# Kernel tuning notes

Measured on AMD Instinct MI355X. Metric: run time of the kernel, lower is better.

## Reference

```python
import jax, jax.numpy as jnp
import numpy as np

B, N, DIM, H = 4, 2048, 1024, 16
HEAD_DIM = DIM // H
SCALE = HEAD_DIM ** -0.5


def setup_inputs() -> dict:
    key = jax.random.key(0)
    k1, k2, k3 = jax.random.split(key, 3)
    x = jax.random.normal(k1, (B, N, DIM), dtype=jnp.float32)
    w_qkv = jax.random.normal(k2, (DIM, 3 * DIM), dtype=jnp.float32) * (DIM ** -0.5)
    w_proj = jax.random.normal(k3, (DIM, DIM), dtype=jnp.float32) * (DIM ** -0.5)
    b_proj = jnp.zeros((DIM,), dtype=jnp.float32)
    return {"x": x, "w_qkv": w_qkv, "w_proj": w_proj, "b_proj": b_proj}


def reference(x, w_qkv, w_proj, b_proj):
    Bs, Ns, C = x.shape
    qkv = x @ w_qkv                       # [B, N, 3C]
    q, k, v = jnp.split(qkv, 3, axis=-1)
    # [B, N, C] -> [B, H, N, D]
    def heads(t):
        return t.reshape(Bs, Ns, H, HEAD_DIM).transpose(0, 2, 1, 3)
    q, k, v = heads(q), heads(k), heads(v)
    attn = jnp.einsum('bhnd,bhmd->bhnm', q, k) * SCALE
    attn = jax.nn.softmax(attn, axis=-1)
    out = jnp.einsum('bhnm,bhmd->bhnd', attn, v)
    out = out.transpose(0, 2, 1, 3).reshape(Bs, Ns, C)
    return out @ w_proj + b_proj
```

## Files before the change

### kernel.cpp

```cpp
#include <hip/hip_runtime.h>
#include <hip/hip_bf16.h>


typedef short bf16x8 __attribute__((ext_vector_type(8)));
typedef float f32x4  __attribute__((ext_vector_type(4)));

#define BN   4
#define SEQ  2048
#define CDIM 1024
#define NH   16
#define HD   64
#define QKVN 3072
#define MTOT 8192
#define QSCALE_LOG2E 0.18033688011112042f

static __device__ __forceinline__ unsigned short f2bf(float f){
    union { float f; unsigned int i; } v; v.f = f;
    unsigned int r = v.i + 0x7FFFu + ((v.i >> 16) & 1u);
    return (unsigned short)(r >> 16);
}

static __device__ __forceinline__ unsigned int pk2bf(float a, float b){
#if __has_builtin(__builtin_amdgcn_cvt_pk_bf16_f32)
    auto r = __builtin_amdgcn_cvt_pk_bf16_f32(a, b);
    unsigned int u; __builtin_memcpy(&u, &r, 4); return u;
#else
    return (unsigned int)f2bf(a) | ((unsigned int)f2bf(b) << 16);
#endif
}

static __device__ __forceinline__ float fast_exp2(float x){
#if __has_builtin(__builtin_amdgcn_exp2f)
    return __builtin_amdgcn_exp2f(x);
#else
    return __expf(x * 0.69314718055994531f);
#endif
}

typedef __attribute__((address_space(3))) unsigned int        as3_uint;
typedef const __attribute__((address_space(1))) unsigned int  as1_uint;
static __device__ __forceinline__ void load_lds16(
    const unsigned short* g, unsigned short* l)
{
    __builtin_amdgcn_global_load_lds((as1_uint*)g, (as3_uint*)l, 16, 0, 0);
}

__global__ __launch_bounds__(256) void convert_f32_bf16(
    const float* __restrict__ in, unsigned short* __restrict__ out)
{
    size_t i = ((size_t)blockIdx.x * 256 + threadIdx.x) * 8;
    f32x4 a = *(const f32x4*)(in + i);
    f32x4 b = *(const f32x4*)(in + i + 4);
    union { unsigned int u[4]; bf16x8 v; } o;
    o.u[0] = pk2bf(a[0], a[1]); o.u[1] = pk2bf(a[2], a[3]);
    o.u[2] = pk2bf(b[0], b[1]); o.u[3] = pk2bf(b[2], b[3]);
    *(bf16x8*)(out + i) = o.v;
}

__global__ __launch_bounds__(256) void transpose_f32_to_bf16(
    const float* __restrict__ in, unsigned short* __restrict__ out,
    int in_rs, int out_rs)
{
    __shared__ unsigned short tile[32][33];
    int c0 = blockIdx.x * 32, r0 = blockIdx.y * 32;
    int tx = threadIdx.x, ty = threadIdx.y;
    #pragma unroll
    for (int j = 0; j < 4; j++)
        tile[ty + 8*j][tx] = f2bf(in[(long long)(r0 + ty + 8*j) * in_rs + c0 + tx]);
    __syncthreads();
    #pragma unroll
    for (int j = 0; j < 4; j++)
        out[(long long)(c0 + ty + 8*j) * out_rs + r0 + tx] = tile[tx][ty + 8*j];
}

__global__ __launch_bounds__(256) void pack_k(
    const unsigned short* __restrict__ qkv, unsigned short* __restrict__ kvpack)
{
    int blk = blockIdx.x;
    int bh = blk >> 6, t = blk & 63;
    int b = bh >> 4, h = bh & 15;
    int tid = threadIdx.x;
    int fr = tid >> 6, l = tid & 63;
    int quad = l >> 4, l15 = l & 15;
    int tb = fr >> 1, d32 = (fr & 1) * 32;
    int row = b*SEQ + t*32 + (l15 >> 2)*8 + (l15 & 3) + 4*tb;
    bf16x8 v = *(const bf16x8*)(qkv + (size_t)row * QKVN + CDIM + h*HD + d32 + quad*8);
    *(bf16x8*)(kvpack + ((size_t)blk*8 + fr)*512 + (size_t)l*8) = v;
}

__global__ __launch_bounds__(256) void pack_v(
    const unsigned short* __restrict__ qkv, unsigned short* __restrict__ vpack)
{
    __shared__ unsigned short tile[32][66];
    int blk = blockIdx.x;
    int bh = blk >> 6, t = blk & 63;
    int b = bh >> 4, h = bh & 15;
    int tid = threadIdx.x;
    int kk = tid >> 3, dd8 = (tid & 7) * 8;
    bf16x8 v = *(const bf16x8*)(qkv + (size_t)(b*SEQ + t*32 + kk) * QKVN
                                + 2*CDIM + h*HD + dd8);
    #pragma unroll
    for (int e = 0; e < 8; e++) tile[kk][dd8 + e] = v[e];
    __syncthreads();
    int db = tid >> 6, quad = (tid >> 4) & 3, l15 = tid & 15;
    bf16x8 o;
    #pragma unroll
    for (int e = 0; e < 8; e++) o[e] = tile[quad*8 + e][db*16 + l15];
    *(bf16x8*)(vpack + ((size_t)blk*8 + 4 + db)*512 + (size_t)(quad*16 + l15)*8) = o;
}

template<bool OUTF32>
__global__ __launch_bounds__(256) void gemm_lds(
    const unsigned short* __restrict__ A,
    const unsigned short* __restrict__ BT,
    void* __restrict__ Cv,
    const float* __restrict__ bias,
    int K, int Cstride, int qcols, float qscale)
{
    __shared__ unsigned short a_lds[128*32];
    __shared__ unsigned short b_lds[128*32];

    int tid  = threadIdx.x;
    int wave = tid >> 6, lane = tid & 63, quad = lane >> 4, l15 = lane & 15;
    int m_blk = blockIdx.y * 128, n_blk = blockIdx.x * 128;

    const unsigned short* ag = A  + (size_t)(m_blk + (tid >> 2)) * K + (tid & 3)*8;
    const unsigned short* bg = BT + (size_t)(n_blk + (tid >> 2)) * K + (tid & 3)*8;
    const size_t row64 = (size_t)64 * K;

    unsigned short* afr = a_lds + ((wave & 1)*64 + l15)*32 + quad*8;
    unsigned short* bfr = b_lds + ((wave >> 1)*64 + l15)*32 + quad*8;

    f32x4 acc[4][4];
    #pragma unroll
    for (int i = 0; i < 4; i++)
        #pragma unroll
        for (int j = 0; j < 4; j++)
            acc[i][j] = f32x4{0.f, 0.f, 0.f, 0.f};

    for (int k0 = 0; k0 < K; k0 += 32) {
        __syncthreads();
        load_lds16(ag,         a_lds + (size_t)tid*8);
        load_lds16(ag + row64, a_lds + 2048 + (size_t)tid*8);
        load_lds16(bg,         b_lds + (size_t)tid*8);
        load_lds16(bg + row64, b_lds + 2048 + (size_t)tid*8);
        ag += 32; bg += 32;
        __syncthreads();

        bf16x8 af[4], bf[4];
        #pragma unroll
        for (int i = 0; i < 4; i++) af[i] = *(const bf16x8*)(afr + 16*i*32);
        #pragma unroll
        for (int i = 0; i < 4; i++) bf[i] = *(const bf16x8*)(bfr + 16*i*32);

        #pragma unroll
        for (int mi = 0; mi < 4; mi++)
            #pragma unroll
            for (int ni = 0; ni < 4; ni++)
                acc[mi][ni] = __builtin_amdgcn_mfma_f32_16x16x32_bf16(
                                  af[mi], bf[ni], acc[mi][ni], 0, 0, 0);
    }

    int m0 = m_blk + (wave & 1) * 64;
    int n0 = n_blk + (wave >> 1) * 64;
    #pragma unroll
    for (int ni = 0; ni < 4; ni++) {
        int col = n0 + 16*ni + l15;
        float bv = bias ? bias[col] : 0.f;
        #pragma unroll
        for (int mi = 0; mi < 4; mi++)
            #pragma unroll
            for (int r = 0; r < 4; r++) {
                int row = m0 + 16*mi + quad*4 + r;
                float v = acc[mi][ni][r] + bv;
                if (col < qcols) v *= qscale;
                if (OUTF32) ((float*)Cv)[(size_t)row * Cstride + col] = v;
                else ((unsigned short*)Cv)[(size_t)row * Cstride + col] = f2bf(v);
            }
    }
}


__global__ __launch_bounds__(256, 4) void attn_kernel(
    const unsigned short* __restrict__ qkv,
    const unsigned short* __restrict__ kvpack,
    unsigned short* __restrict__ ctx)
{
    __shared__ unsigned short kvtile[4][4096];

    int tid  = threadIdx.x;
    int wave = tid >> 6, lane = tid & 63, quad = lane >> 4, l15 = lane & 15;
    int p  = blockIdx.x;
    int L  = (p & 7) * 128 + (p >> 3);
    int bh = L >> 4;
    int rb = L & 15;
    int b = bh >> 4, h = bh & 15;
    int i0 = rb * 128 + wave * 32;

    const unsigned short* qbA =
        qkv + (size_t)(b*SEQ + i0 + l15) * QKVN + h*HD + quad*8;
    const unsigned short* qbB = qbA + (size_t)16 * QKVN;
    bf16x8 qA0 = *(const bf16x8*)(qbA);
    bf16x8 qA1 = *(const bf16x8*)(qbA + 32);
    bf16x8 qB0 = *(const bf16x8*)(qbB);
    bf16x8 qB1 = *(const bf16x8*)(qbB + 32);

    const unsigned short* kvg = kvpack + (size_t)bh * 64 * 4096;

#define STAGE(BUF, T) do {                                                     \
        load_lds16(kvg + (size_t)(T)*4096 + tid*8,        &kvtile[BUF][tid*8]);\
        load_lds16(kvg + (size_t)(T)*4096 + 2048 + tid*8,                      \
                   &kvtile[BUF][2048 + tid*8]);                                \
    } while (0)

#define SYNC(N) do {                                                           \
        __builtin_amdgcn_sched_barrier(0);                                     \
        asm volatile("s_waitcnt vmcnt(" #N ")" ::: "memory");                  \
        __builtin_amdgcn_s_barrier();                                          \
        __builtin_amdgcn_sched_barrier(0);                                     \
    } while (0)

    const f32x4 zf = {0.f, 0.f, 0.f, 0.f};
    f32x4 oA0 = zf, oA1 = zf, oA2 = zf, oA3 = zf;
    f32x4 oB0 = zf, oB1 = zf, oB2 = zf, oB3 = zf;
    f32x4 lA = zf, lB = zf;

    bf16x8 ones;
    #pragma unroll
    for (int e = 0; e < 8; e++) ones[e] = (short)0x3F80;

#define ATTN_TILE(LK)                                                              \
    {                                                                              \
        bf16x8 k0a = *(const bf16x8*)((LK));                                       \
        bf16x8 k0b = *(const bf16x8*)((LK) + 512);                                 \
        bf16x8 k1a = *(const bf16x8*)((LK) + 1024);                                \
        bf16x8 k1b = *(const bf16x8*)((LK) + 1536);                                \
        bf16x8 v0  = *(const bf16x8*)((LK) + 2048);                                \
        bf16x8 v1  = *(const bf16x8*)((LK) + 2560);                                \
        bf16x8 v2  = *(const bf16x8*)((LK) + 3072);                                \
        bf16x8 v3  = *(const bf16x8*)((LK) + 3584);                                \
        f32x4 sA0 = __builtin_amdgcn_mfma_f32_16x16x32_bf16(k0a, qA0, zf, 0,0,0);  \
        sA0 = __builtin_amdgcn_mfma_f32_16x16x32_bf16(k0b, qA1, sA0, 0,0,0);       \
        f32x4 sA1 = __builtin_amdgcn_mfma_f32_16x16x32_bf16(k1a, qA0, zf, 0,0,0);  \
        sA1 = __builtin_amdgcn_mfma_f32_16x16x32_bf16(k1b, qA1, sA1, 0,0,0);       \
        f32x4 sB0 = __builtin_amdgcn_mfma_f32_16x16x32_bf16(k0a, qB0, zf, 0,0,0);  \
        sB0 = __builtin_amdgcn_mfma_f32_16x16x32_bf16(k0b, qB1, sB0, 0,0,0);       \
        f32x4 sB1 = __builtin_amdgcn_mfma_f32_16x16x32_bf16(k1a, qB0, zf, 0,0,0);  \
        sB1 = __builtin_amdgcn_mfma_f32_16x16x32_bf16(k1b, qB1, sB1, 0,0,0);       \
        union { unsigned int u[4]; bf16x8 v; } pkA, pkB;                           \
        pkA.u[0] = pk2bf(fast_exp2(sA0[0]), fast_exp2(sA0[1]));                    \
        pkA.u[1] = pk2bf(fast_exp2(sA0[2]), fast_exp2(sA0[3]));                    \
        pkA.u[2] = pk2bf(fast_exp2(sA1[0]), fast_exp2(sA1[1]));                    \
        pkA.u[3] = pk2bf(fast_exp2(sA1[2]), fast_exp2(sA1[3]));                    \
        pkB.u[0] = pk2bf(fast_exp2(sB0[0]), fast_exp2(sB0[1]));                    \
        pkB.u[1] = pk2bf(fast_exp2(sB0[2]), fast_exp2(sB0[3]));                    \
        pkB.u[2] = pk2bf(fast_exp2(sB1[0]), fast_exp2(sB1[1]));                    \
        pkB.u[3] = pk2bf(fast_exp2(sB1[2]), fast_exp2(sB1[3]));                    \
        lA  = __builtin_amdgcn_mfma_f32_16x16x32_bf16(pkA.v, ones, lA, 0,0,0);     \
        lB  = __builtin_amdgcn_mfma_f32_16x16x32_bf16(pkB.v, ones, lB, 0,0,0);     \
        oA0 = __builtin_amdgcn_mfma_f32_16x16x32_bf16(pkA.v, v0, oA0, 0,0,0);      \
        oA1 = __builtin_amdgcn_mfma_f32_16x16x32_bf16(pkA.v, v1, oA1, 0,0,0);      \
        oA2 = __builtin_amdgcn_mfma_f32_16x16x32_bf16(pkA.v, v2, oA2, 0,0,0);      \
        oA3 = __builtin_amdgcn_mfma_f32_16x16x32_bf16(pkA.v, v3, oA3, 0,0,0);      \
        oB0 = __builtin_amdgcn_mfma_f32_16x16x32_bf16(pkB.v, v0, oB0, 0,0,0);      \
        oB1 = __builtin_amdgcn_mfma_f32_16x16x32_bf16(pkB.v, v1, oB1, 0,0,0);      \
        oB2 = __builtin_amdgcn_mfma_f32_16x16x32_bf16(pkB.v, v2, oB2, 0,0,0);      \
        oB3 = __builtin_amdgcn_mfma_f32_16x16x32_bf16(pkB.v, v3, oB3, 0,0,0);      \
    }

    asm volatile("s_waitcnt vmcnt(0)" ::: "memory");

    STAGE(0, 0); STAGE(1, 1); STAGE(2, 2);

    const unsigned short* lds0 = &kvtile[0][lane*8];

    for (int t = 0; t < 61; ++t) {
        SYNC(4);
        STAGE((t + 3) & 3, t + 3);
        ATTN_TILE(lds0 + (t & 3) * 4096);
    }
    SYNC(4); ATTN_TILE(lds0 + 1 * 4096);
    SYNC(2); ATTN_TILE(lds0 + 2 * 4096);
    SYNC(0); ATTN_TILE(lds0 + 3 * 4096);

    #pragma unroll
    for (int r = 0; r < 4; r++) {
        float invA = 1.f / lA[r];
        float invB = 1.f / lB[r];
        int rowA = b*SEQ + i0 + quad*4 + r;
        size_t baseA = (size_t)rowA * CDIM + h*HD + l15;
        size_t baseB = baseA + (size_t)16 * CDIM;
        ctx[baseA]      = f2bf(oA0[r] * invA);
        ctx[baseA + 16] = f2bf(oA1[r] * invA);
        ctx[baseA + 32] = f2bf(oA2[r] * invA);
        ctx[baseA + 48] = f2bf(oA3[r] * invA);
        ctx[baseB]      = f2bf(oB0[r] * invB);
        ctx[baseB + 16] = f2bf(oB1[r] * invB);
        ctx[baseB + 32] = f2bf(oB2[r] * invB);
        ctx[baseB + 48] = f2bf(oB3[r] * invB);
    }
#undef STAGE
#undef SYNC
#undef ATTN_TILE
}

extern "C" void kernel_launch(void* const* d_in, const int* in_sizes, int n_in,
                              void* d_out, int out_size, void* d_ws, size_t ws_size,
                              hipStream_t stream)
{
    const float* x      = (const float*)d_in[0];
    const float* w_qkv  = (const float*)d_in[1];
    const float* w_proj = (const float*)d_in[2];
    const float* b_proj = (const float*)d_in[3];
    float* out = (float*)d_out;

    char* ws = (char*)d_ws;
    unsigned short* qkv    = (unsigned short*)(ws);
    unsigned short* ctx    = (unsigned short*)(ws + 50331648);
    unsigned short* kvpack = (unsigned short*)(ws + 67108864);
    unsigned short* xb     = (unsigned short*)(ws + 83886080);
    unsigned short* wqkvT  = (unsigned short*)(ws + 100663296);
    unsigned short* wprojT = (unsigned short*)(ws + 106954752);

    dim3 tb(32, 8);
    transpose_f32_to_bf16<<<dim3(QKVN/32, CDIM/32), tb, 0, stream>>>(
        w_qkv, wqkvT, QKVN, CDIM);
    transpose_f32_to_bf16<<<dim3(CDIM/32, CDIM/32), tb, 0, stream>>>(
        w_proj, wprojT, CDIM, CDIM);

    convert_f32_bf16<<<dim3(MTOT*CDIM/2048), 256, 0, stream>>>(x, xb);

    gemm_lds<false><<<dim3(QKVN/128, MTOT/128), 256, 0, stream>>>(
        xb, wqkvT, qkv, nullptr, CDIM, QKVN, CDIM, QSCALE_LOG2E);

    pack_k<<<dim3(64*64), 256, 0, stream>>>(qkv, kvpack);
    pack_v<<<dim3(64*64), 256, 0, stream>>>(qkv, kvpack);

    attn_kernel<<<dim3(BN * NH * (SEQ/128)), 256, 0, stream>>>(
        qkv, kvpack, ctx);

    gemm_lds<true><<<dim3(CDIM/128, MTOT/128), 256, 0, stream>>>(
        ctx, wprojT, out, b_proj, CDIM, CDIM, 0, 1.0f);
}
```

Baseline: 297.2 us.

## Fuse K/V packing into QKV GEMM epilogue and swizzle GEMM block order

The QKV GEMM epilogue now writes K and V directly into the packed attention layout, which removes the separate pack_k and pack_v kernels and their extra read and write of the K/V slices. Both GEMMs switch to a 1D grid with an XCD-aware swizzle so neighbouring tiles share cache. The xb buffer now aliases ctx to save workspace. The fused epilogue uses scattered 2-byte stores for K and 8-byte stores for V, so write coalescing may suffer.

```diff
diff --git a/kernel.cpp b/kernel.cpp
--- a/kernel.cpp
+++ b/kernel.cpp
@@ -73,56 +73,26 @@
         out[(long long)(c0 + ty + 8*j) * out_rs + r0 + tx] = tile[tx][ty + 8*j];
 }
 
-__global__ __launch_bounds__(256) void pack_k(
-    const unsigned short* __restrict__ qkv, unsigned short* __restrict__ kvpack)
-{
-    int blk = blockIdx.x;
-    int bh = blk >> 6, t = blk & 63;
-    int b = bh >> 4, h = bh & 15;
-    int tid = threadIdx.x;
-    int fr = tid >> 6, l = tid & 63;
-    int quad = l >> 4, l15 = l & 15;
-    int tb = fr >> 1, d32 = (fr & 1) * 32;
-    int row = b*SEQ + t*32 + (l15 >> 2)*8 + (l15 & 3) + 4*tb;
-    bf16x8 v = *(const bf16x8*)(qkv + (size_t)row * QKVN + CDIM + h*HD + d32 + quad*8);
-    *(bf16x8*)(kvpack + ((size_t)blk*8 + fr)*512 + (size_t)l*8) = v;
-}
-
-__global__ __launch_bounds__(256) void pack_v(
-    const unsigned short* __restrict__ qkv, unsigned short* __restrict__ vpack)
-{
-    __shared__ unsigned short tile[32][66];
-    int blk = blockIdx.x;
-    int bh = blk >> 6, t = blk & 63;
-    int b = bh >> 4, h = bh & 15;
-    int tid = threadIdx.x;
-    int kk = tid >> 3, dd8 = (tid & 7) * 8;
-    bf16x8 v = *(const bf16x8*)(qkv + (size_t)(b*SEQ + t*32 + kk) * QKVN
-                                + 2*CDIM + h*HD + dd8);
-    #pragma unroll
-    for (int e = 0; e < 8; e++) tile[kk][dd8 + e] = v[e];
-    __syncthreads();
-    int db = tid >> 6, quad = (tid >> 4) & 3, l15 = tid & 15;
-    bf16x8 o;
-    #pragma unroll
-    for (int e = 0; e < 8; e++) o[e] = tile[quad*8 + e][db*16 + l15];
-    *(bf16x8*)(vpack + ((size_t)blk*8 + 4 + db)*512 + (size_t)(quad*16 + l15)*8) = o;
-}
-
-template<bool OUTF32>
+template<int MODE, int NX>
 __global__ __launch_bounds__(256) void gemm_lds(
     const unsigned short* __restrict__ A,
     const unsigned short* __restrict__ BT,
     void* __restrict__ Cv,
+    unsigned short* __restrict__ kvpack,
     const float* __restrict__ bias,
-    int K, int Cstride, int qcols, float qscale)
+    int K, int Cstride)
 {
     __shared__ unsigned short a_lds[128*32];
     __shared__ unsigned short b_lds[128*32];
 
     int tid  = threadIdx.x;
     int wave = tid >> 6, lane = tid & 63, quad = lane >> 4, l15 = lane & 15;
-    int m_blk = blockIdx.y * 128, n_blk = blockIdx.x * 128;
+
+    int nwg = gridDim.x;
+    int cpx = nwg >> 3;
+    int bid = blockIdx.x;
+    int swz = (bid & 7) * cpx + (bid >> 3);
+    int m_blk = (swz / NX) * 128, n_blk = (swz % NX) * 128;
 
     const unsigned short* ag = A  + (size_t)(m_blk + (tid >> 2)) * K + (tid & 3)*8;
     const unsigned short* bg = BT + (size_t)(n_blk + (tid >> 2)) * K + (tid & 3)*8;
@@ -163,20 +133,78 @@
 
     int m0 = m_blk + (wave & 1) * 64;
     int n0 = n_blk + (wave >> 1) * 64;
-    #pragma unroll
-    for (int ni = 0; ni < 4; ni++) {
-        int col = n0 + 16*ni + l15;
-        float bv = bias ? bias[col] : 0.f;
-        #pragma unroll
-        for (int mi = 0; mi < 4; mi++)
-            #pragma unroll
-            for (int r = 0; r < 4; r++) {
-                int row = m0 + 16*mi + quad*4 + r;
-                float v = acc[mi][ni][r] + bv;
-                if (col < qcols) v *= qscale;
-                if (OUTF32) ((float*)Cv)[(size_t)row * Cstride + col] = v;
-                else ((unsigned short*)Cv)[(size_t)row * Cstride + col] = f2bf(v);
+
+    if constexpr (MODE == 0) {
+        float* C = (float*)Cv;
+        #pragma unroll
+        for (int ni = 0; ni < 4; ni++) {
+            int col = n0 + 16*ni + l15;
+            float bv = bias ? bias[col] : 0.f;
+            #pragma unroll
+            for (int mi = 0; mi < 4; mi++)
+                #pragma unroll
+                for (int r = 0; r < 4; r++) {
+                    int row = m0 + 16*mi + quad*4 + r;
+                    C[(size_t)row * Cstride + col] = acc[mi][ni][r] + bv;
+                }
+        }
+    } else {
+        unsigned short* qkvo = (unsigned short*)Cv;
+        int rg = n0 >> 10;
+        if (rg == 0) {
+            #pragma unroll
+            for (int ni = 0; ni < 4; ni++) {
+                int col = n0 + 16*ni + l15;
+                #pragma unroll
+                for (int mi = 0; mi < 4; mi++)
+                    #pragma unroll
+                    for (int r = 0; r < 4; r++) {
+                        int row = m0 + 16*mi + quad*4 + r;
+                        qkvo[(size_t)row * Cstride + col] =
+                            f2bf(acc[mi][ni][r] * QSCALE_LOG2E);
+                    }
             }
+        } else if (rg == 1) {
+            #pragma unroll
+            for (int ni = 0; ni < 4; ni++) {
+                int col = n0 + 16*ni + l15 - 1024;
+                int h = col >> 6, d = col & 63;
+                int quadd = (d & 31) >> 3, e = d & 7, dhi = d >> 5;
+                #pragma unroll
+                for (int mi = 0; mi < 4; mi++)
+                    #pragma unroll
+                    for (int r = 0; r < 4; r++) {
+                        int row = m0 + 16*mi + quad*4 + r;
+                        int b = row >> 11, t = (row & 2047) >> 5, key = row & 31;
+                        int tb = (key >> 2) & 1;
+                        int l15a = ((key >> 3) << 2) + (key & 3);
+                        size_t addr =
+                            ((size_t)(((b*16 + h)*64 + t)*8 + tb*2 + dhi))*512
+                            + (size_t)(quadd*16 + l15a)*8 + e;
+                        kvpack[addr] = f2bf(acc[mi][ni][r]);
+                    }
+            }
+        } else {
+            #pragma unroll
+            for (int ni = 0; ni < 4; ni++) {
+                int col = n0 + 16*ni + l15 - 2048;
+                int h = col >> 6, d = col & 63;
+                int db = d >> 4, l15v = d & 15;
+                #pragma unroll
+                for (int mi = 0; mi < 4; mi++) {
+                    int row0 = m0 + 16*mi + quad*4;
+                    int b = row0 >> 11, t = (row0 & 2047) >> 5, key0 = row0 & 31;
+                    int quadv = key0 >> 3, e0 = key0 & 7;
+                    size_t addr =
+                        ((size_t)(((b*16 + h)*64 + t)*8 + 4 + db))*512
+                        + (size_t)(quadv*16 + l15v)*8 + e0;
+                    union { unsigned int u[2]; unsigned long long ull; } o;
+                    o.u[0] = pk2bf(acc[mi][ni][0], acc[mi][ni][1]);
+                    o.u[1] = pk2bf(acc[mi][ni][2], acc[mi][ni][3]);
+                    *(unsigned long long*)(kvpack + addr) = o.ull;
+                }
+            }
+        }
     }
 }
 
@@ -317,8 +345,8 @@
     char* ws = (char*)d_ws;
     unsigned short* qkv    = (unsigned short*)(ws);
     unsigned short* ctx    = (unsigned short*)(ws + 50331648);
+    unsigned short* xb     = ctx;
     unsigned short* kvpack = (unsigned short*)(ws + 67108864);
-    unsigned short* xb     = (unsigned short*)(ws + 83886080);
     unsigned short* wqkvT  = (unsigned short*)(ws + 100663296);
     unsigned short* wprojT = (unsigned short*)(ws + 106954752);
 
@@ -330,15 +358,12 @@
 
     convert_f32_bf16<<<dim3(MTOT*CDIM/2048), 256, 0, stream>>>(x, xb);
 
-    gemm_lds<false><<<dim3(QKVN/128, MTOT/128), 256, 0, stream>>>(
-        xb, wqkvT, qkv, nullptr, CDIM, QKVN, CDIM, QSCALE_LOG2E);
-
-    pack_k<<<dim3(64*64), 256, 0, stream>>>(qkv, kvpack);
-    pack_v<<<dim3(64*64), 256, 0, stream>>>(qkv, kvpack);
+    gemm_lds<1, QKVN/128><<<dim3((QKVN/128)*(MTOT/128)), 256, 0, stream>>>(
+        xb, wqkvT, qkv, kvpack, nullptr, CDIM, QKVN);
 
     attn_kernel<<<dim3(BN * NH * (SEQ/128)), 256, 0, stream>>>(
         qkv, kvpack, ctx);
 
-    gemm_lds<true><<<dim3(CDIM/128, MTOT/128), 256, 0, stream>>>(
-        ctx, wprojT, out, b_proj, CDIM, CDIM, 0, 1.0f);
-}
+    gemm_lds<0, CDIM/128><<<dim3((CDIM/128)*(MTOT/128)), 256, 0, stream>>>(
+        ctx, wprojT, out, nullptr, b_proj, CDIM, CDIM);
+}
```

After: 276.6 us. 6.9% less time.
